# Performance work log

Measured on AMD Instinct MI355X. Metric: run time of the kernel, lower is better.

The kernel has to match this reference:

```python
import jax, jax.numpy as jnp
import numpy as np

HID = 2048; H = 16; QLR = 1536; KVLR = 512
DN = 128; DR = 64; DV = 128; DQ = DN + DR  # 192
B = 2; S = 2048
THETA = 10000.0; EPS = 1e-6


def rms_norm(x, w, eps=EPS):
    x32 = x.astype(jnp.float32)
    var = jnp.mean(x32 * x32, axis=-1, keepdims=True)
    return (w * (x32 * jax.lax.rsqrt(var + eps))).astype(x.dtype)


def rotate_half(x):
    x1, x2 = jnp.split(x, 2, axis=-1)
    return jnp.concatenate((-x2, x1), axis=-1)


def rope_tables(seq_len, dim, base=THETA):
    inv_freq = 1.0 / (base ** (jnp.arange(0, dim, 2, dtype=jnp.float32) / dim))
    t = jnp.arange(seq_len, dtype=jnp.float32)
    freqs = jnp.outer(t, inv_freq)            # [S, dim/2]
    emb = jnp.concatenate((freqs, freqs), -1)  # [S, dim]
    return jnp.cos(emb), jnp.sin(emb)


def setup_inputs() -> dict:
    key = jax.random.key(0)
    ks = jax.random.split(key, 8)
    sd = lambda fan_in: 1.0 / np.sqrt(fan_in)
    return {
        "hidden_states": jax.random.normal(ks[0], (B, S, HID), jnp.float32),
        "w_qa": jax.random.normal(ks[1], (QLR, HID), jnp.float32) * sd(HID),
        "q_a_ln_w": jnp.ones((QLR,), jnp.float32),
        "w_qb": jax.random.normal(ks[2], (H * DQ, QLR), jnp.float32) * sd(QLR),
        "w_kva": jax.random.normal(ks[3], (KVLR + DR, HID), jnp.float32) * sd(HID),
        "kv_a_ln_w": jnp.ones((KVLR,), jnp.float32),
        "w_kvb": jax.random.normal(ks[4], (H * (DN + DV), KVLR), jnp.float32) * sd(KVLR),
        "w_o": jax.random.normal(ks[5], (HID, H * DV), jnp.float32) * sd(H * DV),
    }


def reference(hidden_states, w_qa, q_a_ln_w, w_qb, w_kva, kv_a_ln_w, w_kvb, w_o):
    b, s, _ = hidden_states.shape
    scale = DQ ** -0.5
    cos, sin = rope_tables(s, DR)  # [S, DR] each

    # Q path: low-rank down-proj -> RMSNorm -> up-proj
    cq = rms_norm(hidden_states @ w_qa.T, q_a_ln_w)            # [B,S,QLR]
    q = (cq @ w_qb.T).reshape(b, s, H, DQ).transpose(0, 2, 1, 3)  # [B,H,S,DQ]
    q_nope, q_pe = q[..., :DN], q[..., DN:]
    q_pe = q_pe * cos + rotate_half(q_pe) * sin

    # KV path: joint compressed kv + shared rope key
    ckv = hidden_states @ w_kva.T                               # [B,S,KVLR+DR]
    k_pe = ckv[..., KVLR:].reshape(b, s, 1, DR).transpose(0, 2, 1, 3)  # [B,1,S,DR]
    k_pe = k_pe * cos + rotate_half(k_pe) * sin
    ckv_l = rms_norm(ckv[..., :KVLR], kv_a_ln_w)                # [B,S,KVLR]
    kv = (ckv_l @ w_kvb.T).reshape(b, s, H, DN + DV).transpose(0, 2, 1, 3)
    k_nope, v = kv[..., :DN], kv[..., DN:]                      # [B,H,S,DN],[B,H,S,DV]

    q_full = jnp.concatenate([q_nope, q_pe], axis=-1)           # [B,H,S,DQ]
    k_full = jnp.concatenate(
        [k_nope, jnp.broadcast_to(k_pe, (b, H, s, DR))], axis=-1)

    scores = jnp.einsum('bhqd,bhkd->bhqk', q_full, k_full) * scale
    causal = jnp.triu(jnp.ones((s, s), dtype=bool), k=1)
    scores = jnp.where(causal, -jnp.inf, scores)
    attn = jax.nn.softmax(scores.astype(jnp.float32), axis=-1).astype(q_full.dtype)

    out = jnp.einsum('bhqk,bhkd->bhqd', attn, v)                # [B,H,S,DV]
    out = out.transpose(0, 2, 1, 3).reshape(b, s, H * DV)
    return out @ w_o.T
```

## Files before the change

### kernel.cpp

```cpp
#include <hip/hip_runtime.h>
#include <stdint.h>
#include <stddef.h>

typedef unsigned short u16;
typedef short s16x8 __attribute__((ext_vector_type(8)));
typedef unsigned short u16x4 __attribute__((ext_vector_type(4)));
typedef unsigned short u16x8 __attribute__((ext_vector_type(8)));
typedef float f32x4 __attribute__((ext_vector_type(4)));

__device__ __forceinline__ u16 f2b(float f) {
  uint32_t u = __builtin_bit_cast(uint32_t, f);
  uint32_t r = u + 0x7fffu + ((u >> 16) & 1u);
  return (u16)(r >> 16);
}
__device__ __forceinline__ float b2f(u16 h) {
  uint32_t u = ((uint32_t)h) << 16;
  return __builtin_bit_cast(float, u);
}
__device__ __forceinline__ void gl_lds16(const void* g, void* l) {
  __builtin_amdgcn_global_load_lds((const __attribute__((address_space(1))) void*)g,
                                   (__attribute__((address_space(3))) void*)l,
                                   16, 0, 0);
}

__global__ __launch_bounds__(256) void cast_k(const float* __restrict__ in,
                                              u16* __restrict__ out, int n4) {
  int i = blockIdx.x * 256 + threadIdx.x;
  if (i >= n4) return;
  float4 v = ((const float4*)in)[i];
  u16x4 o; o[0]=f2b(v.x); o[1]=f2b(v.y); o[2]=f2b(v.z); o[3]=f2b(v.w);
  ((u16x4*)out)[i] = o;
}

__global__ __launch_bounds__(256) void cast_pad_k(const float* __restrict__ in,
                                                  u16* __restrict__ out,
                                                  int Kd, int nvalid, int n4) {
  int i = blockIdx.x * 256 + threadIdx.x;
  if (i >= n4) return;
  int row = (i << 2) / Kd;
  u16x4 o;
  if (row < nvalid) {
    float4 v = ((const float4*)in)[i];
    o[0]=f2b(v.x); o[1]=f2b(v.y); o[2]=f2b(v.z); o[3]=f2b(v.w);
  } else {
    o[0]=0; o[1]=0; o[2]=0; o[3]=0;
  }
  ((u16x4*)out)[i] = o;
}

template<int MODE>
__global__ __launch_bounds__(256) void gemm_bt(const u16* __restrict__ A,
                                               const u16* __restrict__ B,
                                               void* __restrict__ Cv,
                                               int M, int N, int K) {
  __shared__ u16 As[128 * 32];
  __shared__ u16 Bs[128 * 32];
  const int t = threadIdx.x;
  const int w = t >> 6, l = t & 63;
  const int nb = N >> 7;
  const int cpx = gridDim.x >> 3;
  const int swz = (blockIdx.x & 7) * cpx + (blockIdx.x >> 3);
  const int bm = (swz / nb) << 7;
  const int bn = (swz % nb) << 7;
  const int wr = (w >> 1) << 6;
  const int wc = (w & 1) << 6;

  f32x4 acc[4][4];
  #pragma unroll
  for (int i = 0; i < 4; i++)
    #pragma unroll
    for (int j = 0; j < 4; j++) acc[i][j] = (f32x4){0.f, 0.f, 0.f, 0.f};

  const u16* ga = A + (size_t)(bm + w * 32 + (l >> 2)) * K + ((l & 3) * 8);
  const u16* gb = B + (size_t)(bn + w * 32 + (l >> 2)) * K + ((l & 3) * 8);
  u16* la0 = &As[(w * 32) * 32];
  u16* la1 = &As[(w * 32 + 16) * 32];
  u16* lb0 = &Bs[(w * 32) * 32];
  u16* lb1 = &Bs[(w * 32 + 16) * 32];

  for (int k0 = 0; k0 < K; k0 += 32) {
    __syncthreads();
    gl_lds16(ga, la0);
    gl_lds16(ga + (size_t)16 * K, la1);
    gl_lds16(gb, lb0);
    gl_lds16(gb + (size_t)16 * K, lb1);
    ga += 32; gb += 32;
    __syncthreads();

    s16x8 af[4], bf[4];
    #pragma unroll
    for (int i = 0; i < 4; i++) {
      af[i] = *(const s16x8*)&As[(wr + i * 16 + (l & 15)) * 32 + (l >> 4) * 8];
      bf[i] = *(const s16x8*)&Bs[(wc + i * 16 + (l & 15)) * 32 + (l >> 4) * 8];
    }
    #pragma unroll
    for (int mi = 0; mi < 4; mi++)
      #pragma unroll
      for (int ni = 0; ni < 4; ni++)
        acc[mi][ni] = __builtin_amdgcn_mfma_f32_16x16x32_bf16(af[mi], bf[ni], acc[mi][ni], 0, 0, 0);
  }

  #pragma unroll
  for (int mi = 0; mi < 4; mi++)
    #pragma unroll
    for (int ni = 0; ni < 4; ni++) {
      int row0 = bm + wr + mi * 16 + ((l >> 4) << 2);
      int col  = bn + wc + ni * 16 + (l & 15);
      #pragma unroll
      for (int r = 0; r < 4; r++) {
        float v = acc[mi][ni][r];
        size_t idx = (size_t)(row0 + r) * N + col;
        if (MODE == 1) ((u16*)Cv)[idx] = f2b(v);
        else           ((float*)Cv)[idx] = v;
      }
    }
}

__global__ __launch_bounds__(256) void rmsnorm_k(const float* __restrict__ X,
                                                 const float* __restrict__ W,
                                                 u16* __restrict__ Y, int ldx, int D) {
  const int row = blockIdx.x;
  const float* x = X + (size_t)row * ldx;
  const int t = threadIdx.x;
  float ss = 0.f;
  for (int i = t; i < (D >> 2); i += 256) {
    float4 v = ((const float4*)x)[i];
    ss += v.x * v.x + v.y * v.y + v.z * v.z + v.w * v.w;
  }
  #pragma unroll
  for (int off = 32; off > 0; off >>= 1) ss += __shfl_xor(ss, off);
  __shared__ float red[4];
  if ((t & 63) == 0) red[t >> 6] = ss;
  __syncthreads();
  float tot = red[0] + red[1] + red[2] + red[3];
  float r = rsqrtf(tot / (float)D + 1e-6f);
  u16* y = Y + (size_t)row * D;
  for (int i = t; i < (D >> 2); i += 256) {
    float4 v = ((const float4*)x)[i];
    float4 g = ((const float4*)W)[i];
    u16x4 o;
    o[0] = f2b(v.x * r * g.x); o[1] = f2b(v.y * r * g.y);
    o[2] = f2b(v.z * r * g.z); o[3] = f2b(v.w * r * g.w);
    ((u16x4*)y)[i] = o;
  }
}

__global__ __launch_bounds__(256) void rope_kpe_k(const float* __restrict__ CQ,
                                                  u16* __restrict__ Kpe) {
  int idx = blockIdx.x * 256 + threadIdx.x;
  if (idx >= 4096 * 32) return;
  int d = idx & 31;
  int m = idx >> 5;
  int s = m & 2047;
  float inv = expf(-(float)(2 * d) * (9.210340371976184f / 64.0f));
  float ang = (float)s * inv;
  float sn, c;
  sincosf(ang, &sn, &c);
  float x1 = CQ[(size_t)m * 2176 + 2048 + d];
  float x2 = CQ[(size_t)m * 2176 + 2080 + d];
  Kpe[m * 64 + d]      = f2b(x1 * c - x2 * sn);
  Kpe[m * 64 + 32 + d] = f2b(x2 * c + x1 * sn);
}

__global__ __launch_bounds__(256) void rope_q_k(u16* __restrict__ Qb) {
  int idx = blockIdx.x * 256 + threadIdx.x;
  if (idx >= 4096 * 16 * 32) return;
  int d = idx & 31;
  int h = (idx >> 5) & 15;
  int m = idx >> 9;
  int s = m & 2047;
  float inv = expf(-(float)(2 * d) * (9.210340371976184f / 64.0f));
  float ang = (float)s * inv;
  float sn, c;
  sincosf(ang, &sn, &c);
  size_t base = (size_t)m * 3072 + h * 192 + 128 + d;
  float x1 = b2f(Qb[base]);
  float x2 = b2f(Qb[base + 32]);
  Qb[base]      = f2b(x1 * c - x2 * sn);
  Qb[base + 32] = f2b(x2 * c + x1 * sn);
}

__global__ __launch_bounds__(256) void vt_k(const u16* __restrict__ KV,
                                            u16* __restrict__ VT) {
  __shared__ u16 L[64][72];
  const int t = threadIdx.x;
  const int s_t = blockIdx.x & 31;
  const int d_t = (blockIdx.x >> 5) & 1;
  const int bh  = blockIdx.x >> 6;
  const int h = bh & 15, b = bh >> 4;
  const size_t bS = (size_t)b * 2048;
  const int s0 = s_t << 6, d0 = d_t << 6;

  #pragma unroll
  for (int i = 0; i < 2; i++) {
    int rs = (t >> 3) + i * 32;
    int ch = t & 7;
    u16x8 v = *(const u16x8*)&KV[(bS + s0 + rs) * 4096 + h * 256 + 128 + d0 + ch * 8];
    *(u16x8*)&L[rs][ch * 8] = v;
  }
  __syncthreads();
  #pragma unroll
  for (int i = 0; i < 2; i++) {
    int rd = (t >> 3) + i * 32;
    int ch = t & 7;
    u16x8 o;
    #pragma unroll
    for (int j = 0; j < 8; j++) o[j] = L[ch * 8 + j][rd];
    *(u16x8*)&VT[((size_t)bh * 128 + d0 + rd) * 2048 + s0 + ch * 8] = o;
  }
}

__global__ __launch_bounds__(256, 4) void attn5_k(const u16* __restrict__ Q,
                                                  const u16* __restrict__ KV,
                                                  const u16* __restrict__ Kpe,
                                                  const u16* __restrict__ VT,
                                                  u16* __restrict__ O) {
  const float SCALE = 0.07216878364870322f;
  const int t = threadIdx.x, w = t >> 6, l = t & 63;
  const int bh = blockIdx.x & 31;
  const int qt = 31 - (blockIdx.x >> 5);
  const int h = bh & 15, b = bh >> 4;
  const int q0 = qt << 6;
  const size_t bS = (size_t)b * 2048;

  __shared__ u16 Kn[2][32 * 128];
  __shared__ u16 Kp[2][32 * 64];
  __shared__ u16 Pl[4][16][40];

  s16x8 qf[6];
  {
    const u16* qp = Q + (bS + q0 + w * 16 + (l & 15)) * 3072 + h * 192 + ((l >> 4) * 8);
    #pragma unroll
    for (int c = 0; c < 6; c++) qf[c] = *(const s16x8*)(qp + c * 32);
  }
  float m_i[4] = {-1e30f, -1e30f, -1e30f, -1e30f};
  float lp[4]  = {0.f, 0.f, 0.f, 0.f};
  f32x4 accO[8];
  #pragma unroll
  for (int i = 0; i < 8; i++) accO[i] = (f32x4){0.f, 0.f, 0.f, 0.f};

  const u16* vbp = VT + (size_t)bh * 128 * 2048;
  const int ktiles = (q0 >> 5) + 2;

  auto STAGE = [&](int buf, int k0) {
    #pragma unroll
    for (int it = 0; it < 2; ++it) {
      int r = it * 16 + w * 4 + (l >> 4);
      int g = (l & 15) ^ (r & 7);
      gl_lds16(KV + (bS + k0 + r) * 4096 + h * 256 + g * 8,
               &Kn[buf][(it * 256 + w * 64) * 8]);
    }
    {
      int r = w * 8 + (l >> 3);
      int g = (l & 7) ^ (r & 7);
      gl_lds16(Kpe + (bS + k0 + r) * 64 + g * 8, &Kp[buf][(w * 64) * 8]);
    }
  };

  STAGE(0, 0);
  __syncthreads();

  int cur = 0;
  for (int kt = 0; kt < ktiles; ++kt) {
    const int k0 = kt << 5;

    s16x8 va[8];
    #pragma unroll
    for (int df = 0; df < 8; df++)
      va[df] = *(const s16x8*)&vbp[(size_t)(df * 16 + (l & 15)) * 2048 + k0 + (l >> 4) * 8];

    if (kt + 1 < ktiles) STAGE(cur ^ 1, k0 + 32);

    f32x4 sa[2];
    sa[0] = (f32x4){0.f, 0.f, 0.f, 0.f};
    sa[1] = (f32x4){0.f, 0.f, 0.f, 0.f};
    #pragma unroll
    for (int c = 0; c < 4; c++) {
      #pragma unroll
      for (int cf = 0; cf < 2; cf++) {
        int row = cf * 16 + (l & 15);
        int ch = (c * 4 + (l >> 4)) ^ (row & 7);
        s16x8 kf = *(const s16x8*)&Kn[cur][row * 128 + ch * 8];
        sa[cf] = __builtin_amdgcn_mfma_f32_16x16x32_bf16(qf[c], kf, sa[cf], 0, 0, 0);
      }
    }
    #pragma unroll
    for (int c = 4; c < 6; c++) {
      #pragma unroll
      for (int cf = 0; cf < 2; cf++) {
        int row = cf * 16 + (l & 15);
        int ch = ((c - 4) * 4 + (l >> 4)) ^ (row & 7);
        s16x8 kf = *(const s16x8*)&Kp[cur][row * 64 + ch * 8];
        sa[cf] = __builtin_amdgcn_mfma_f32_16x16x32_bf16(qf[c], kf, sa[cf], 0, 0, 0);
      }
    }

    #pragma unroll
    for (int cf = 0; cf < 2; cf++)
      #pragma unroll
      for (int r = 0; r < 4; r++) sa[cf][r] *= SCALE;
    if (k0 + 32 > q0 + w * 16) {
      #pragma unroll
      for (int cf = 0; cf < 2; cf++)
        #pragma unroll
        for (int r = 0; r < 4; r++) {
          int qrow = q0 + w * 16 + ((l >> 4) << 2) + r;
          if (k0 + cf * 16 + (l & 15) > qrow) sa[cf][r] = -1e30f;
        }
    }

    float lm[4];
    #pragma unroll
    for (int r = 0; r < 4; r++) lm[r] = fmaxf(sa[0][r], sa[1][r]);
    bool safe = (lm[0] <= m_i[0] + 8.f) && (lm[1] <= m_i[1] + 8.f) &&
                (lm[2] <= m_i[2] + 8.f) && (lm[3] <= m_i[3] + 8.f);
    if (!__all(safe)) {
      #pragma unroll
      for (int r = 0; r < 4; r++) {
        float mx = lm[r];
        #pragma unroll
        for (int dd = 1; dd < 16; dd <<= 1) mx = fmaxf(mx, __shfl_xor(mx, dd));
        float mnew = fmaxf(m_i[r], mx);
        float alpha = __expf(m_i[r] - mnew);
        m_i[r] = mnew;
        lp[r] *= alpha;
        #pragma unroll
        for (int df = 0; df < 8; df++) accO[df][r] *= alpha;
      }
    }
    #pragma unroll
    for (int r = 0; r < 4; r++) {
      float e0 = __expf(sa[0][r] - m_i[r]);
      float e1 = __expf(sa[1][r] - m_i[r]);
      lp[r] += e0 + e1;
      int prow = ((l >> 4) << 2) + r;
      Pl[w][prow][(l & 15)]      = f2b(e0);
      Pl[w][prow][16 + (l & 15)] = f2b(e1);
    }

    {
      s16x8 pf = *(const s16x8*)&Pl[w][l & 15][(l >> 4) * 8];
      #pragma unroll
      for (int df = 0; df < 8; df++)
        accO[df] = __builtin_amdgcn_mfma_f32_16x16x32_bf16(pf, va[df], accO[df], 0, 0, 0);
    }

    __syncthreads();
    cur ^= 1;
  }

  #pragma unroll
  for (int r = 0; r < 4; r++) {
    float s = lp[r];
    #pragma unroll
    for (int dd = 1; dd < 16; dd <<= 1) s += __shfl_xor(s, dd);
    float rl = 1.0f / s;
    #pragma unroll
    for (int df = 0; df < 8; df++) {
      float o = accO[df][r] * rl;
      O[(bS + q0 + w * 16 + ((l >> 4) << 2) + r) * 2048 + h * 128 + df * 16 + (l & 15)] = f2b(o);
    }
  }
}

extern "C" void kernel_launch(void* const* d_in, const int* in_sizes, int n_in,
                              void* d_out, int out_size, void* d_ws, size_t ws_size,
                              hipStream_t stream) {
  const float* hs    = (const float*)d_in[0];
  const float* w_qa  = (const float*)d_in[1];
  const float* q_ln  = (const float*)d_in[2];
  const float* w_qb  = (const float*)d_in[3];
  const float* w_kva = (const float*)d_in[4];
  const float* kv_ln = (const float*)d_in[5];
  const float* w_kvb = (const float*)d_in[6];
  const float* w_o   = (const float*)d_in[7];
  float* out = (float*)d_out;

  char* ws = (char*)d_ws;
  size_t off = 0;
  auto alloc = [&](size_t bytes) -> void* {
    void* p = ws + off;
    off = (off + bytes + 255) & ~(size_t)255;
    return p;
  };
  u16* Xb     = (u16*)alloc(4096ull * 2048 * 2);
  u16* Wcat   = (u16*)alloc(2176ull * 2048 * 2);
  u16* Wqb    = (u16*)alloc(3072ull * 1536 * 2);
  u16* Wkvb   = (u16*)alloc(4096ull * 512 * 2);
  u16* Wo     = (u16*)alloc(2048ull * 2048 * 2);
  float* CQcat = (float*)alloc(4096ull * 2176 * 4);
  u16* CQn    = (u16*)alloc(4096ull * 1536 * 2);
  u16* CKVn   = (u16*)alloc(4096ull * 512 * 2);
  u16* Kpe    = (u16*)alloc(4096ull * 64 * 2);
  u16* KVb    = (u16*)alloc(4096ull * 4096 * 2);
  u16* Ob     = (u16*)alloc(4096ull * 2048 * 2);
  u16* Qb     = (u16*)CQcat;
  u16* VT     = Xb;

  cast_k<<<dim3(8192), 256, 0, stream>>>(hs, Xb, 8388608 / 4);
  cast_k<<<dim3(3072), 256, 0, stream>>>(w_qa, Wcat, 3145728 / 4);
  cast_pad_k<<<dim3(1280), 256, 0, stream>>>(w_kva, Wcat + 1536ull * 2048, 2048, 576, 1310720 / 4);
  cast_k<<<dim3(4608), 256, 0, stream>>>(w_qb, Wqb, 4718592 / 4);
  cast_k<<<dim3(2048), 256, 0, stream>>>(w_kvb, Wkvb, 2097152 / 4);
  cast_k<<<dim3(4096), 256, 0, stream>>>(w_o, Wo, 4194304 / 4);

  gemm_bt<0><<<dim3(32 * 17), 256, 0, stream>>>(Xb, Wcat, CQcat, 4096, 2176, 2048);

  rmsnorm_k<<<dim3(4096), 256, 0, stream>>>(CQcat, q_ln, CQn, 2176, 1536);
  rmsnorm_k<<<dim3(4096), 256, 0, stream>>>(CQcat + 1536, kv_ln, CKVn, 2176, 512);
  rope_kpe_k<<<dim3(512), 256, 0, stream>>>(CQcat, Kpe);

  gemm_bt<1><<<dim3(32 * 24), 256, 0, stream>>>(CQn, Wqb, Qb, 4096, 3072, 1536);
  gemm_bt<1><<<dim3(32 * 32), 256, 0, stream>>>(CKVn, Wkvb, KVb, 4096, 4096, 512);
  rope_q_k<<<dim3(8192), 256, 0, stream>>>(Qb);

  vt_k<<<dim3(32 * 2 * 32), 256, 0, stream>>>(KVb, VT);

  attn5_k<<<dim3(32 * 32), 256, 0, stream>>>(Qb, KVb, Kpe, VT, Ob);

  gemm_bt<0><<<dim3(32 * 16), 256, 0, stream>>>(Ob, Wo, out, 4096, 2048, 2048);
}
```

Measured before the change: 619.2 us.

## Load K fragments directly from global memory instead of LDS double-buffering

The attention kernel no longer stages K and rotary-K tiles into shared memory with async global-to-LDS copies and double buffering. Each wave now loads its K fragments straight from global memory into registers, which removes the per-iteration block barrier and the LDS footprint. The trade-off is that all four waves load the same K rows redundantly and the accesses are strided, relying on L1/L2 hits. The launch-bounds occupancy hint is also dropped.

```diff
diff --git a/kernel.cpp b/kernel.cpp
--- a/kernel.cpp
+++ b/kernel.cpp
@@ -210,11 +210,11 @@
   }
 }
 
-__global__ __launch_bounds__(256, 4) void attn5_k(const u16* __restrict__ Q,
-                                                  const u16* __restrict__ KV,
-                                                  const u16* __restrict__ Kpe,
-                                                  const u16* __restrict__ VT,
-                                                  u16* __restrict__ O) {
+__global__ __launch_bounds__(256) void attn6_k(const u16* __restrict__ Q,
+                                               const u16* __restrict__ KV,
+                                               const u16* __restrict__ Kpe,
+                                               const u16* __restrict__ VT,
+                                               u16* __restrict__ O) {
   const float SCALE = 0.07216878364870322f;
   const int t = threadIdx.x, w = t >> 6, l = t & 63;
   const int bh = blockIdx.x & 31;
@@ -223,8 +223,6 @@
   const int q0 = qt << 6;
   const size_t bS = (size_t)b * 2048;
 
-  __shared__ u16 Kn[2][32 * 128];
-  __shared__ u16 Kp[2][32 * 64];
   __shared__ u16 Pl[4][16][40];
 
   s16x8 qf[6];
@@ -240,27 +238,10 @@
   for (int i = 0; i < 8; i++) accO[i] = (f32x4){0.f, 0.f, 0.f, 0.f};
 
   const u16* vbp = VT + (size_t)bh * 128 * 2048;
+  const u16* kbp = KV + (bS) * 4096 + h * 256;
+  const u16* pbp = Kpe + (bS) * 64;
   const int ktiles = (q0 >> 5) + 2;
 
-  auto STAGE = [&](int buf, int k0) {
-    #pragma unroll
-    for (int it = 0; it < 2; ++it) {
-      int r = it * 16 + w * 4 + (l >> 4);
-      int g = (l & 15) ^ (r & 7);
-      gl_lds16(KV + (bS + k0 + r) * 4096 + h * 256 + g * 8,
-               &Kn[buf][(it * 256 + w * 64) * 8]);
-    }
-    {
-      int r = w * 8 + (l >> 3);
-      int g = (l & 7) ^ (r & 7);
-      gl_lds16(Kpe + (bS + k0 + r) * 64 + g * 8, &Kp[buf][(w * 64) * 8]);
-    }
-  };
-
-  STAGE(0, 0);
-  __syncthreads();
-
-  int cur = 0;
   for (int kt = 0; kt < ktiles; ++kt) {
     const int k0 = kt << 5;
 
@@ -268,31 +249,27 @@
     #pragma unroll
     for (int df = 0; df < 8; df++)
       va[df] = *(const s16x8*)&vbp[(size_t)(df * 16 + (l & 15)) * 2048 + k0 + (l >> 4) * 8];
-
-    if (kt + 1 < ktiles) STAGE(cur ^ 1, k0 + 32);
 
     f32x4 sa[2];
     sa[0] = (f32x4){0.f, 0.f, 0.f, 0.f};
     sa[1] = (f32x4){0.f, 0.f, 0.f, 0.f};
     #pragma unroll
-    for (int c = 0; c < 4; c++) {
-      #pragma unroll
-      for (int cf = 0; cf < 2; cf++) {
-        int row = cf * 16 + (l & 15);
-        int ch = (c * 4 + (l >> 4)) ^ (row & 7);
-        s16x8 kf = *(const s16x8*)&Kn[cur][row * 128 + ch * 8];
-        sa[cf] = __builtin_amdgcn_mfma_f32_16x16x32_bf16(qf[c], kf, sa[cf], 0, 0, 0);
-      }
-    }
-    #pragma unroll
-    for (int c = 4; c < 6; c++) {
-      #pragma unroll
-      for (int cf = 0; cf < 2; cf++) {
-        int row = cf * 16 + (l & 15);
-        int ch = ((c - 4) * 4 + (l >> 4)) ^ (row & 7);
-        s16x8 kf = *(const s16x8*)&Kp[cur][row * 64 + ch * 8];
-        sa[cf] = __builtin_amdgcn_mfma_f32_16x16x32_bf16(qf[c], kf, sa[cf], 0, 0, 0);
-      }
+    for (int cf = 0; cf < 2; cf++) {
+      const int krow = k0 + cf * 16 + (l & 15);
+      const u16* kr = kbp + (size_t)krow * 4096 + (l >> 4) * 8;
+      const u16* pr = pbp + (size_t)krow * 64 + (l >> 4) * 8;
+      s16x8 kf0 = *(const s16x8*)(kr);
+      s16x8 kf1 = *(const s16x8*)(kr + 32);
+      s16x8 kf2 = *(const s16x8*)(kr + 64);
+      s16x8 kf3 = *(const s16x8*)(kr + 96);
+      s16x8 kf4 = *(const s16x8*)(pr);
+      s16x8 kf5 = *(const s16x8*)(pr + 32);
+      sa[cf] = __builtin_amdgcn_mfma_f32_16x16x32_bf16(qf[0], kf0, sa[cf], 0, 0, 0);
+      sa[cf] = __builtin_amdgcn_mfma_f32_16x16x32_bf16(qf[1], kf1, sa[cf], 0, 0, 0);
+      sa[cf] = __builtin_amdgcn_mfma_f32_16x16x32_bf16(qf[2], kf2, sa[cf], 0, 0, 0);
+      sa[cf] = __builtin_amdgcn_mfma_f32_16x16x32_bf16(qf[3], kf3, sa[cf], 0, 0, 0);
+      sa[cf] = __builtin_amdgcn_mfma_f32_16x16x32_bf16(qf[4], kf4, sa[cf], 0, 0, 0);
+      sa[cf] = __builtin_amdgcn_mfma_f32_16x16x32_bf16(qf[5], kf5, sa[cf], 0, 0, 0);
     }
 
     #pragma unroll
@@ -344,9 +321,6 @@
       for (int df = 0; df < 8; df++)
         accO[df] = __builtin_amdgcn_mfma_f32_16x16x32_bf16(pf, va[df], accO[df], 0, 0, 0);
     }
-
-    __syncthreads();
-    cur ^= 1;
   }
 
   #pragma unroll
@@ -416,7 +390,7 @@
 
   vt_k<<<dim3(32 * 2 * 32), 256, 0, stream>>>(KVb, VT);
 
-  attn5_k<<<dim3(32 * 32), 256, 0, stream>>>(Qb, KVb, Kpe, VT, Ob);
+  attn6_k<<<dim3(32 * 32), 256, 0, stream>>>(Qb, KVb, Kpe, VT, Ob);
 
   gemm_bt<0><<<dim3(32 * 16), 256, 0, stream>>>(Ob, Wo, out, 4096, 2048, 2048);
 }
```

Measured after the change: 698.5 us. +12.8%, slower.
